# Optimization experiments

Hardware: AMD Instinct MI355X
Metric: run time of the kernel (lower is better)

Reference implementation:

```python
import jax, jax.numpy as jnp
import numpy as np

N = 8192          # num atoms
APM = 32          # atoms per molecule
M = N // APM      # 256 molecules
FEAT = 100        # hidden_channels == num_filters
NG = 25           # num gaussians
K = 28            # knn neighbors
L = 4             # num interaction blocks
CUTOFF = 6.0
LOG2 = float(np.log(2.0))


def ssp(x):
    # pyg ShiftedSoftplus: softplus(x) - log(2)
    return jax.nn.softplus(x) - LOG2


def setup_inputs() -> dict:
    key = jax.random.key(0)
    ks = jax.random.split(key, 16)
    z = jax.random.randint(ks[0], (N,), 1, 100)
    pos = jax.random.normal(ks[1], (N, 3), jnp.float32) * 2.0
    ptr = jnp.arange(0, N + APM, APM)  # [M+1] molecule boundaries

    def w(k, shape, fan):
        return (jax.random.normal(k, shape, jnp.float32) / np.sqrt(fan)).astype(jnp.float32)

    def b(k, shape):
        return jax.random.normal(k, shape, jnp.float32) * 0.01

    kb = jax.random.split(ks[15], 8)
    H = FEAT // 2
    return {
        "z": z,
        "pos": pos,
        "ptr": ptr,
        "emb": jax.random.normal(ks[2], (100, FEAT), jnp.float32),
        "mlp_w1": w(ks[3], (L, NG, FEAT), NG),
        "mlp_b1": b(kb[0], (L, FEAT)),
        "mlp_w2": w(ks[4], (L, FEAT, FEAT), FEAT),
        "mlp_b2": b(kb[1], (L, FEAT)),
        "lin1_w": w(ks[5], (L, FEAT, FEAT), FEAT),
        "lin2_w": w(ks[6], (L, FEAT, FEAT), FEAT),
        "lin2_b": b(kb[2], (L, FEAT)),
        "lin_w": w(ks[7], (L, FEAT, FEAT), FEAT),
        "lin_b": b(kb[3], (L, FEAT)),
        "out_w1": w(ks[8], (FEAT, H), FEAT),
        "out_b1": b(kb[4], (H,)),
        "out_w2": w(ks[9], (H, 1), H),
        "out_b2": b(kb[5], (1,)),
    }


def reference(z, pos, ptr, emb, mlp_w1, mlp_b1, mlp_w2, mlp_b2,
              lin1_w, lin2_w, lin2_b, lin_w, lin_b,
              out_w1, out_b1, out_w2, out_b2):
    n = z.shape[0]
    m = ptr.shape[0] - 1

    # ptr -> per-atom batch ids (index_fill + cumsum; OOB index N dropped)
    flag = jnp.zeros((n,), jnp.int32).at[ptr].set(1, mode="drop")
    flag = flag.at[0].set(0)
    batch = jnp.cumsum(flag)

    # ---- KNN interaction graph (full NxN pairwise distances + masking + topk)
    diff = pos[:, None, :] - pos[None, :, :]           # [N,N,3]
    d2 = jnp.sum(diff * diff, axis=-1)                  # [N,N]
    ar = jnp.arange(n)
    mask = (ar[:, None] == ar[None, :]) \
         | (batch[:, None] != batch[None, :]) \
         | (d2 > CUTOFF * CUTOFF)
    dist = jnp.where(mask, CUTOFF, jnp.sqrt(jnp.where(mask, 1.0, d2)))
    neg, idx = jax.lax.top_k(-dist, K)                  # k nearest per row
    ew = -neg.reshape(-1)                               # edge distances [N*K]
    src = idx.reshape(-1)                               # source atoms j; target of edge (i,m) is i

    # ---- Gaussian smearing
    offset = jnp.linspace(0.0, CUTOFF, NG)
    coeff = -0.5 / (offset[1] - offset[0]) ** 2
    ea = jnp.exp(coeff * (ew[:, None] - offset[None, :]) ** 2)  # [E,NG]

    # cosine cutoff (zero weight for padded edges at dist==cutoff)
    ccut = 0.5 * (jnp.cos(ew * jnp.pi / CUTOFF) + 1.0)          # [E]

    h = emb[z]                                                   # [N,F]
    f = h.shape[1]
    for l in range(L):
        # filter network on edge attributes
        Wf = ssp(ea @ mlp_w1[l] + mlp_b1[l]) @ mlp_w2[l] + mlp_b2[l]
        Wf = Wf * ccut[:, None]                                  # [E,F]
        # CFConv: lin1 -> gather*filter -> sum over k neighbors -> lin2
        x1 = h @ lin1_w[l]                                       # [N,F]
        msg = x1[src] * Wf                                       # [E,F]
        agg = msg.reshape(n, K, f).sum(axis=1)                   # each node i has exactly K incoming edges
        v = ssp(agg @ lin2_w[l] + lin2_b[l]) @ lin_w[l] + lin_b[l]
        h = h + v

    # readout head
    h = ssp(h @ out_w1 + out_b1)
    per_atom = (h @ out_w2 + out_b2).reshape(-1)                 # [N]
    return jax.ops.segment_sum(per_atom, batch, num_segments=m) # per-molecule energy [M]
```

## Files before the change

### kernel.cpp

```cpp
#include <hip/hip_runtime.h>
#include <math.h>

#define APM   32
#define NMOL  256
#define FEAT  100
#define NPAD  112
#define LAYERS 4
#define NTHREADS 1024
#define NWAVES   16
#define G_TBL 1024
#define TSTR  128
#define X1STR 132

typedef _Float16 f16x8 __attribute__((ext_vector_type(8)));
typedef float    f32x4 __attribute__((ext_vector_type(4)));

#define L1F_OFF 0
#define L2F_OFF 14336
#define LVF_OFF 28672
#define LWTOT   43008
#define WTOTAL  (4*LWTOT)

__device__ __forceinline__ float sspf(float x){
  return __logf(1.0f + __expf(x)) - 0.69314718056f;
}

__global__ __launch_bounds__(256) void prep_weights(
    const float* __restrict__ lin1_w, const float* __restrict__ lin2_w,
    const float* __restrict__ lin_w,  _Float16* __restrict__ out)
{
  int gid = blockIdx.x*256 + threadIdx.x;
  int l = gid / LWTOT;
  int r = gid - l*LWTOT;
  const float* W; int e;
  if (r < 14336)      { W = lin1_w + l*10000; e = r; }
  else if (r < 28672) { W = lin2_w + l*10000; e = r - 14336; }
  else                { W = lin_w  + l*10000; e = r - 28672; }
  int j = e & 7, L = (e >> 3) & 63, tile = e >> 9;
  int kc = tile / 7, nt = tile - kc*7;
  int k = kc*32 + ((L >> 4) << 3) + j;
  int f = nt*16 + (L & 15);
  float v = (k < 100 && f < FEAT) ? W[k*FEAT + f] : 0.0f;
  out[gid] = (_Float16)v;
}

__global__ __launch_bounds__(256) void build_table(
    const float* __restrict__ mlp_w1, const float* __restrict__ mlp_b1,
    const float* __restrict__ mlp_w2, const float* __restrict__ mlp_b2,
    float* __restrict__ tbl)
{
  __shared__ float sT[4][100];
  int wv = threadIdx.x >> 6, lane = threadIdx.x & 63;
  int l = blockIdx.x >> 8;
  int s = (blockIdx.x & 255)*4 + wv;
  float d = 6.0f * (float)s / (float)(G_TBL - 1);
  float ea[25];
  #pragma unroll
  for (int g = 0; g < 25; g++){
    float u = d - 0.25f*(float)g;
    ea[g] = __expf(-8.0f*u*u);
  }
  #pragma unroll
  for (int kk = 0; kk < 2; kk++){
    int k = lane + kk*64;
    if (k < 100){
      float acc = mlp_b1[l*100 + k];
      #pragma unroll
      for (int g = 0; g < 25; g++)
        acc += ea[g] * mlp_w1[(l*25 + g)*100 + k];
      sT[wv][k] = sspf(acc);
    }
  }
  float cc = 0.5f*(__cosf(d*0.52359877559f) + 1.0f);
  #pragma unroll
  for (int ff = 0; ff < 2; ff++){
    int f = lane + ff*64;
    float o = 0.0f;
    if (f < 100){
      o = mlp_b2[l*100 + f];
      for (int k = 0; k < 100; k++)
        o += sT[wv][k] * mlp_w2[(l*100 + k)*100 + f];
      o *= cc;
    }
    tbl[((size_t)l*G_TBL + s)*TSTR + f] = o;
  }
}

__device__ __forceinline__ void cpw(_Float16* dst, const _Float16* src, int n16){
  const uint4* s = (const uint4*)src;
  uint4* d = (uint4*)dst;
  for (int i = threadIdx.x; i < n16; i += NTHREADS) d[i] = s[i];
}

__global__ __launch_bounds__(1024)
__attribute__((amdgpu_waves_per_eu(4, 4)))
void schnet_mega(
    const int* __restrict__ z, const float* __restrict__ pos,
    const float* __restrict__ emb, const _Float16* __restrict__ wf,
    const float* __restrict__ tbl,
    const float* __restrict__ lin2_b, const float* __restrict__ lin_b,
    const float* __restrict__ out_w1, const float* __restrict__ out_b1,
    const float* __restrict__ out_w2, const float* __restrict__ out_b2,
    float* __restrict__ out)
{
  __shared__ __align__(16) _Float16 sWA[28672];
  __shared__ __align__(16) _Float16 sAf[APM*136];
  __shared__ __align__(16) _Float16 sBf[APM*136];
  __shared__ __align__(16) float    sX1[APM*X1STR];
  __shared__ __align__(16) float    sH [APM*NPAD];
  __shared__ float sD [APM*33];
  __shared__ float sM [APM*33];
  __shared__ float sB2l[NPAD], sBlv[NPAD];
  __shared__ float sPos[APM*3];
  __shared__ float sPart[NWAVES];

  int tid = threadIdx.x, lane = tid & 63, wv = tid >> 6;
  int q = lane >> 4, n = lane & 15;
  int mol = blockIdx.x, mb = mol*APM;

  if (tid < 96) sPos[tid] = pos[mb*3 + tid];
  if (tid < 512){
    int r0 = tid >> 4, c0 = 112 + (tid & 15);
    sBf[r0*136 + c0] = (_Float16)0.0f;
  }
  for (int i = tid; i < APM*NPAD; i += NTHREADS){
    int r = i/NPAD, c = i - r*NPAD;
    sH[i] = (c < FEAT) ? emb[z[mb+r]*FEAT + c] : 0.0f;
  }
  __syncthreads();
  for (int p = tid; p < APM*APM; p += NTHREADS){
    int i = p >> 5, j = p & 31;
    float dx = sPos[i*3+0]-sPos[j*3+0];
    float dy = sPos[i*3+1]-sPos[j*3+1];
    float dz = sPos[i*3+2]-sPos[j*3+2];
    float d2 = dx*dx + dy*dy + dz*dz;
    float d = (d2 > 36.0f) ? 6.0f : sqrtf(d2);
    sD[i*33+j] = d;
    sM[i*33+j] = 1.0f;
  }
  __syncthreads();
  if (tid < APM){
    float dd[32];
    #pragma unroll
    for (int j = 0; j < 32; j++) dd[j] = sD[tid*33+j];
    dd[tid] = 1e30f;
    unsigned dropped = 0u;
    for (int rr = 0; rr < 4; rr++){
      float mx = -1.0f; int mj = 0;
      #pragma unroll
      for (int j = 0; j < 32; j++){
        bool ok = !((dropped>>j)&1u) && (dd[j] > mx);
        mx = ok ? dd[j] : mx;  mj = ok ? j : mj;
      }
      dropped |= 1u << mj;
    }
    #pragma unroll
    for (int j = 0; j < 32; j++)
      if ((dropped>>j)&1u) sM[tid*33+j] = 0.0f;
  }
  __syncthreads();

  for (int l = 0; l < LAYERS; l++){
    const _Float16* wl = wf + l*LWTOT;
    const float* tb = tbl + (size_t)l*G_TBL*TSTR;
    cpw(sWA, wl + L1F_OFF, 14336/8);
    if (tid < 224){
      int w = tid/112, i = tid - w*112;
      float v = (i < FEAT) ? (w==0 ? lin2_b : lin_b)[l*FEAT + i] : 0.0f;
      (w==0 ? sB2l : sBlv)[i] = v;
    }
    for (int i = tid; i < APM*128; i += NTHREADS){
      int r = i >> 7, c = i & 127;
      sAf[r*136+c] = (c < NPAD) ? (_Float16)sH[r*NPAD+c] : (_Float16)0.0f;
    }
    __syncthreads();
    for (int tau = wv; tau < 14; tau += NWAVES){
      int mt = tau/7, nt = tau - mt*7;
      f32x4 acc = {0.0f,0.0f,0.0f,0.0f};
      #pragma unroll
      for (int kc = 0; kc < 4; kc++){
        f16x8 a = *(const f16x8*)&sAf[(mt*16+n)*136 + kc*32 + q*8];
        f16x8 b = *(const f16x8*)&sWA[((kc*7+nt)*64 + lane)*8];
        acc = __builtin_amdgcn_mfma_f32_16x16x32_f16(a, b, acc, 0, 0, 0);
      }
      #pragma unroll
      for (int r = 0; r < 4; r++)
        sX1[(mt*16+q*4+r)*X1STR + nt*16+n] = acc[r];
    }
    __syncthreads();
    cpw(sWA, wl + L2F_OFF, 28672/8);
    {
      #pragma unroll 1
      for (int t = 0; t < 2; t++){
        int a = wv*2 + t;
        int f0 = lane, f1 = lane + 64;
        float agg0 = 0.0f, agg1 = 0.0f;
        #pragma unroll 1
        for (int j0 = 0; j0 < 32; j0 += 4){
          float w00[4], w01[4], w10[4], w11[4], frv[4], mv[4];
          #pragma unroll
          for (int u = 0; u < 4; u++){
            int j = j0 + u;
            float d = sD[a*33+j];
            mv[u] = sM[a*33+j];
            float un = d * (float)((G_TBL-1)/6.0);
            int s = (int)un;
            s = (s > G_TBL-2) ? (G_TBL-2) : s;
            frv[u] = un - (float)s;
            const float* rp = tb + s*TSTR;
            w00[u] = rp[f0]; w01[u] = rp[TSTR+f0];
            w10[u] = rp[f1]; w11[u] = rp[TSTR+f1];
          }
          #pragma unroll
          for (int u = 0; u < 4; u++){
            int j = j0 + u;
            float wa = w00[u] + frv[u]*(w01[u]-w00[u]);
            float wb = w10[u] + frv[u]*(w11[u]-w10[u]);
            agg0 += (mv[u]*wa) * sX1[j*X1STR + f0];
            agg1 += (mv[u]*wb) * sX1[j*X1STR + f1];
          }
        }
        sAf[a*136 + f0] = (_Float16)agg0;
        sAf[a*136 + f1] = (_Float16)agg1;
      }
    }
    __syncthreads();
    for (int tau = wv; tau < 14; tau += NWAVES){
      int mt = tau/7, nt = tau - mt*7;
      f32x4 acc = {0.0f,0.0f,0.0f,0.0f};
      #pragma unroll
      for (int kc = 0; kc < 4; kc++){
        f16x8 a = *(const f16x8*)&sAf[(mt*16+n)*136 + kc*32 + q*8];
        f16x8 b = *(const f16x8*)&sWA[((kc*7+nt)*64 + lane)*8];
        acc = __builtin_amdgcn_mfma_f32_16x16x32_f16(a, b, acc, 0, 0, 0);
      }
      float bb = sB2l[nt*16+n];
      #pragma unroll
      for (int r = 0; r < 4; r++)
        sBf[(mt*16+q*4+r)*136 + nt*16+n] = (_Float16)sspf(acc[r] + bb);
    }
    __syncthreads();
    for (int tau = wv; tau < 14; tau += NWAVES){
      int mt = tau/7, nt = tau - mt*7;
      f32x4 acc = {0.0f,0.0f,0.0f,0.0f};
      #pragma unroll
      for (int kc = 0; kc < 4; kc++){
        f16x8 a = *(const f16x8*)&sBf[(mt*16+n)*136 + kc*32 + q*8];
        f16x8 b = *(const f16x8*)&sWA[14336 + ((kc*7+nt)*64 + lane)*8];
        acc = __builtin_amdgcn_mfma_f32_16x16x32_f16(a, b, acc, 0, 0, 0);
      }
      int f = nt*16 + n;
      if (f < FEAT){
        float bb = sBlv[f];
        #pragma unroll
        for (int r = 0; r < 4; r++)
          sH[(mt*16+q*4+r)*NPAD + f] += acc[r] + bb;
      }
    }
    __syncthreads();
  }

  float* rw = (float*)sWA;
  for (int i = tid; i < 5000; i += NTHREADS) rw[i] = out_w1[i];
  if (tid < 50){ sB2l[tid] = out_b1[tid]; sBlv[tid] = out_w2[tid]; }
  __syncthreads();
  float ob2 = out_b2[0];
  float partial = 0.0f;
  for (int t = 0; t < 2; t++){
    int a = wv*2 + t;
    float u = 0.0f;
    if (lane < 50){
      u = sB2l[lane];
      #pragma unroll 4
      for (int c = 0; c < FEAT; c++)
        u += sH[a*NPAD + c] * rw[c*50 + lane];
      u = sspf(u) * sBlv[lane];
    }
    #pragma unroll
    for (int s = 1; s < 64; s <<= 1) u += __shfl_xor(u, s);
    partial += u + ob2;
  }
  if (lane == 0) sPart[wv] = partial;
  __syncthreads();
  if (tid == 0){
    float s = 0.0f;
    #pragma unroll
    for (int i = 0; i < NWAVES; i++) s += sPart[i];
    out[mol] = s;
  }
}

extern "C" void kernel_launch(void* const* d_in, const int* in_sizes, int n_in,
                              void* d_out, int out_size, void* d_ws, size_t ws_size,
                              hipStream_t stream)
{
  const int*   z      = (const int*)  d_in[0];
  const float* pos    = (const float*)d_in[1];
  const float* emb    = (const float*)d_in[3];
  const float* mlp_w1 = (const float*)d_in[4];
  const float* mlp_b1 = (const float*)d_in[5];
  const float* mlp_w2 = (const float*)d_in[6];
  const float* mlp_b2 = (const float*)d_in[7];
  const float* lin1_w = (const float*)d_in[8];
  const float* lin2_w = (const float*)d_in[9];
  const float* lin2_b = (const float*)d_in[10];
  const float* lin_w  = (const float*)d_in[11];
  const float* lin_b  = (const float*)d_in[12];
  const float* out_w1 = (const float*)d_in[13];
  const float* out_b1 = (const float*)d_in[14];
  const float* out_w2 = (const float*)d_in[15];
  const float* out_b2 = (const float*)d_in[16];

  _Float16* wfrag = (_Float16*)d_ws;
  float*    tbl   = (float*)((char*)d_ws + WTOTAL*2);

  prep_weights<<<WTOTAL/256, 256, 0, stream>>>(lin1_w, lin2_w, lin_w, wfrag);
  build_table<<<4*(G_TBL/4), 256, 0, stream>>>(mlp_w1, mlp_b1, mlp_w2, mlp_b2,
                                               tbl);
  schnet_mega<<<NMOL, NTHREADS, 0, stream>>>(z, pos, emb, wfrag, tbl,
      lin2_b, lin_b, out_w1, out_b1, out_w2, out_b2, (float*)d_out);
}
```

Measured before the change: 166.1 us.

## Merge prep kernels, stage MLP weights in LDS, vectorize edge aggregation, drop mask array

The two setup kernels become one launch, and the filter-table builder loads mlp_w1/mlp_w2 into shared memory once per block, where before every thread read them from global memory. In the main kernel the neighbor mask is folded into the distance array by setting dropped edges to the cutoff distance, where the table value is zero. The aggregation loop processes two features per lane with float2 loads, and the fp16 copy of h is written in the layer epilogue instead of in a separate conversion pass. All three weight matrices share one enlarged LDS buffer, which raises shared-memory use per block.

```diff
diff --git a/kernel.cpp b/kernel.cpp
--- a/kernel.cpp
+++ b/kernel.cpp
@@ -13,7 +13,9 @@
 #define X1STR 132
 
 typedef _Float16 f16x8 __attribute__((ext_vector_type(8)));
+typedef _Float16 f16x2 __attribute__((ext_vector_type(2)));
 typedef float    f32x4 __attribute__((ext_vector_type(4)));
+typedef float    f32x2 __attribute__((ext_vector_type(2)));
 
 #define L1F_OFF 0
 #define L2F_OFF 14336
@@ -21,68 +23,83 @@
 #define LWTOT   43008
 #define WTOTAL  (4*LWTOT)
 
+#define PREP_BLOCKS 672
+#define TBL_BLOCKS  128
+
 __device__ __forceinline__ float sspf(float x){
   return __logf(1.0f + __expf(x)) - 0.69314718056f;
 }
 
-__global__ __launch_bounds__(256) void prep_weights(
+__global__ __launch_bounds__(256) void prep_all(
     const float* __restrict__ lin1_w, const float* __restrict__ lin2_w,
-    const float* __restrict__ lin_w,  _Float16* __restrict__ out)
-{
-  int gid = blockIdx.x*256 + threadIdx.x;
-  int l = gid / LWTOT;
-  int r = gid - l*LWTOT;
-  const float* W; int e;
-  if (r < 14336)      { W = lin1_w + l*10000; e = r; }
-  else if (r < 28672) { W = lin2_w + l*10000; e = r - 14336; }
-  else                { W = lin_w  + l*10000; e = r - 28672; }
-  int j = e & 7, L = (e >> 3) & 63, tile = e >> 9;
-  int kc = tile / 7, nt = tile - kc*7;
-  int k = kc*32 + ((L >> 4) << 3) + j;
-  int f = nt*16 + (L & 15);
-  float v = (k < 100 && f < FEAT) ? W[k*FEAT + f] : 0.0f;
-  out[gid] = (_Float16)v;
-}
-
-__global__ __launch_bounds__(256) void build_table(
+    const float* __restrict__ lin_w,
     const float* __restrict__ mlp_w1, const float* __restrict__ mlp_b1,
     const float* __restrict__ mlp_w2, const float* __restrict__ mlp_b2,
-    float* __restrict__ tbl)
+    _Float16* __restrict__ outw, float* __restrict__ tbl)
 {
+  if (blockIdx.x < PREP_BLOCKS){
+    int gid = blockIdx.x*256 + threadIdx.x;
+    int l = gid / LWTOT;
+    int r = gid - l*LWTOT;
+    const float* W; int e;
+    if (r < 14336)      { W = lin1_w + l*10000; e = r; }
+    else if (r < 28672) { W = lin2_w + l*10000; e = r - 14336; }
+    else                { W = lin_w  + l*10000; e = r - 28672; }
+    int j = e & 7, L = (e >> 3) & 63, tile = e >> 9;
+    int kc = tile / 7, nt = tile - kc*7;
+    int k = kc*32 + ((L >> 4) << 3) + j;
+    int f = nt*16 + (L & 15);
+    float v = (k < 100 && f < FEAT) ? W[k*FEAT + f] : 0.0f;
+    outw[gid] = (_Float16)v;
+    return;
+  }
+  __shared__ float sW2[10000];
+  __shared__ float sW1[2500];
+  __shared__ float sB1[100], sB2[100];
   __shared__ float sT[4][100];
-  int wv = threadIdx.x >> 6, lane = threadIdx.x & 63;
-  int l = blockIdx.x >> 8;
-  int s = (blockIdx.x & 255)*4 + wv;
-  float d = 6.0f * (float)s / (float)(G_TBL - 1);
-  float ea[25];
-  #pragma unroll
-  for (int g = 0; g < 25; g++){
-    float u = d - 0.25f*(float)g;
-    ea[g] = __expf(-8.0f*u*u);
-  }
-  #pragma unroll
-  for (int kk = 0; kk < 2; kk++){
-    int k = lane + kk*64;
-    if (k < 100){
-      float acc = mlp_b1[l*100 + k];
-      #pragma unroll
-      for (int g = 0; g < 25; g++)
-        acc += ea[g] * mlp_w1[(l*25 + g)*100 + k];
-      sT[wv][k] = sspf(acc);
-    }
-  }
-  float cc = 0.5f*(__cosf(d*0.52359877559f) + 1.0f);
-  #pragma unroll
-  for (int ff = 0; ff < 2; ff++){
-    int f = lane + ff*64;
-    float o = 0.0f;
-    if (f < 100){
-      o = mlp_b2[l*100 + f];
-      for (int k = 0; k < 100; k++)
-        o += sT[wv][k] * mlp_w2[(l*100 + k)*100 + f];
-      o *= cc;
-    }
-    tbl[((size_t)l*G_TBL + s)*TSTR + f] = o;
+  int bid = blockIdx.x - PREP_BLOCKS;
+  int l = bid >> 5;
+  int s0 = (bid & 31) * 32;
+  int tid = threadIdx.x, wv = tid >> 6, lane = tid & 63;
+  for (int i = tid; i < 10000; i += 256) sW2[i] = mlp_w2[l*10000 + i];
+  for (int i = tid; i < 2500;  i += 256) sW1[i] = mlp_w1[l*2500 + i];
+  if (tid < 100) sB1[tid] = mlp_b1[l*100 + tid];
+  if (tid >= 128 && tid < 228) sB2[tid-128] = mlp_b2[l*100 + tid-128];
+  __syncthreads();
+  #pragma unroll 1
+  for (int si = 0; si < 8; si++){
+    int s = s0 + wv*8 + si;
+    float d = 6.0f * (float)s / (float)(G_TBL - 1);
+    float ea[25];
+    #pragma unroll
+    for (int g = 0; g < 25; g++){
+      float u = d - 0.25f*(float)g;
+      ea[g] = __expf(-8.0f*u*u);
+    }
+    #pragma unroll
+    for (int kk = 0; kk < 2; kk++){
+      int k = lane + kk*64;
+      if (k < 100){
+        float acc = sB1[k];
+        #pragma unroll
+        for (int g = 0; g < 25; g++)
+          acc += ea[g] * sW1[g*100 + k];
+        sT[wv][k] = sspf(acc);
+      }
+    }
+    float cc = 0.5f*(__cosf(d*0.52359877559f) + 1.0f);
+    #pragma unroll
+    for (int ff = 0; ff < 2; ff++){
+      int f = lane + ff*64;
+      float o = 0.0f;
+      if (f < 100){
+        o = sB2[f];
+        for (int k = 0; k < 100; k++)
+          o += sT[wv][k] * sW2[k*100 + f];
+        o *= cc;
+      }
+      tbl[((size_t)l*G_TBL + s)*TSTR + f] = o;
+    }
   }
 }
 
@@ -103,13 +120,12 @@
     const float* __restrict__ out_w2, const float* __restrict__ out_b2,
     float* __restrict__ out)
 {
-  __shared__ __align__(16) _Float16 sWA[28672];
+  __shared__ __align__(16) _Float16 sWA[43008];
   __shared__ __align__(16) _Float16 sAf[APM*136];
   __shared__ __align__(16) _Float16 sBf[APM*136];
   __shared__ __align__(16) float    sX1[APM*X1STR];
   __shared__ __align__(16) float    sH [APM*NPAD];
   __shared__ float sD [APM*33];
-  __shared__ float sM [APM*33];
   __shared__ float sB2l[NPAD], sBlv[NPAD];
   __shared__ float sPos[APM*3];
   __shared__ float sPart[NWAVES];
@@ -123,9 +139,16 @@
     int r0 = tid >> 4, c0 = 112 + (tid & 15);
     sBf[r0*136 + c0] = (_Float16)0.0f;
   }
-  for (int i = tid; i < APM*NPAD; i += NTHREADS){
-    int r = i/NPAD, c = i - r*NPAD;
-    sH[i] = (c < FEAT) ? emb[z[mb+r]*FEAT + c] : 0.0f;
+  if (tid >= 512 && tid < 512 + APM*20){
+    int i = tid - 512;
+    int r = i/20, c = 112 + (i - r*20);
+    sX1[r*X1STR + c] = 0.0f;
+  }
+  for (int i = tid; i < APM*136; i += NTHREADS){
+    int r = i/136, c = i - r*136;
+    float v = (c < FEAT) ? emb[z[mb+r]*FEAT + c] : 0.0f;
+    sAf[i] = (_Float16)v;
+    if (c < NPAD) sH[r*NPAD + c] = v;
   }
   __syncthreads();
   for (int p = tid; p < APM*APM; p += NTHREADS){
@@ -134,9 +157,7 @@
     float dy = sPos[i*3+1]-sPos[j*3+1];
     float dz = sPos[i*3+2]-sPos[j*3+2];
     float d2 = dx*dx + dy*dy + dz*dz;
-    float d = (d2 > 36.0f) ? 6.0f : sqrtf(d2);
-    sD[i*33+j] = d;
-    sM[i*33+j] = 1.0f;
+    sD[i*33+j] = (d2 > 36.0f) ? 6.0f : sqrtf(d2);
   }
   __syncthreads();
   if (tid < APM){
@@ -156,7 +177,7 @@
     }
     #pragma unroll
     for (int j = 0; j < 32; j++)
-      if ((dropped>>j)&1u) sM[tid*33+j] = 0.0f;
+      if ((dropped>>j)&1u) sD[tid*33+j] = 6.0f;
   }
   __syncthreads();
 
@@ -169,10 +190,6 @@
       float v = (i < FEAT) ? (w==0 ? lin2_b : lin_b)[l*FEAT + i] : 0.0f;
       (w==0 ? sB2l : sBlv)[i] = v;
     }
-    for (int i = tid; i < APM*128; i += NTHREADS){
-      int r = i >> 7, c = i & 127;
-      sAf[r*136+c] = (c < NPAD) ? (_Float16)sH[r*NPAD+c] : (_Float16)0.0f;
-    }
     __syncthreads();
     for (int tau = wv; tau < 14; tau += NWAVES){
       int mt = tau/7, nt = tau - mt*7;
@@ -188,40 +205,41 @@
         sX1[(mt*16+q*4+r)*X1STR + nt*16+n] = acc[r];
     }
     __syncthreads();
-    cpw(sWA, wl + L2F_OFF, 28672/8);
+    cpw(sWA + 14336, wl + L2F_OFF, 28672/8);
     {
+      int fb = 2*lane;
+      const float* rpb = tb + fb;
       #pragma unroll 1
       for (int t = 0; t < 2; t++){
         int a = wv*2 + t;
-        int f0 = lane, f1 = lane + 64;
-        float agg0 = 0.0f, agg1 = 0.0f;
-        #pragma unroll 1
-        for (int j0 = 0; j0 < 32; j0 += 4){
-          float w00[4], w01[4], w10[4], w11[4], frv[4], mv[4];
-          #pragma unroll
-          for (int u = 0; u < 4; u++){
-            int j = j0 + u;
-            float d = sD[a*33+j];
-            mv[u] = sM[a*33+j];
-            float un = d * (float)((G_TBL-1)/6.0);
-            int s = (int)un;
-            s = (s > G_TBL-2) ? (G_TBL-2) : s;
-            frv[u] = un - (float)s;
-            const float* rp = tb + s*TSTR;
-            w00[u] = rp[f0]; w01[u] = rp[TSTR+f0];
-            w10[u] = rp[f1]; w11[u] = rp[TSTR+f1];
+        if (lane < 56){
+          f32x2 agg = {0.0f, 0.0f};
+          #pragma unroll 1
+          for (int j0 = 0; j0 < 32; j0 += 4){
+            float frv[4]; f32x2 w0[4], w1[4];
+            #pragma unroll
+            for (int u = 0; u < 4; u++){
+              float d = sD[a*33 + j0 + u];
+              float un = d * (float)((G_TBL-1)/6.0);
+              int s = (int)un;
+              s = (s > G_TBL-2) ? (G_TBL-2) : s;
+              frv[u] = un - (float)s;
+              const float* rp = rpb + s*TSTR;
+              w0[u] = *(const f32x2*)rp;
+              w1[u] = *(const f32x2*)(rp + TSTR);
+            }
+            #pragma unroll
+            for (int u = 0; u < 4; u++){
+              f32x2 w = w0[u] + frv[u]*(w1[u] - w0[u]);
+              f32x2 x = *(const f32x2*)&sX1[(j0+u)*X1STR + fb];
+              agg += w * x;
+            }
           }
-          #pragma unroll
-          for (int u = 0; u < 4; u++){
-            int j = j0 + u;
-            float wa = w00[u] + frv[u]*(w01[u]-w00[u]);
-            float wb = w10[u] + frv[u]*(w11[u]-w10[u]);
-            agg0 += (mv[u]*wa) * sX1[j*X1STR + f0];
-            agg1 += (mv[u]*wb) * sX1[j*X1STR + f1];
-          }
+          *(f16x2*)&sAf[a*136 + fb] =
+              (f16x2){(_Float16)agg.x, (_Float16)agg.y};
+        } else {
+          *(f16x2*)&sAf[a*136 + fb] = (f16x2){(_Float16)0.0f, (_Float16)0.0f};
         }
-        sAf[a*136 + f0] = (_Float16)agg0;
-        sAf[a*136 + f1] = (_Float16)agg1;
       }
     }
     __syncthreads();
@@ -231,7 +249,7 @@
       #pragma unroll
       for (int kc = 0; kc < 4; kc++){
         f16x8 a = *(const f16x8*)&sAf[(mt*16+n)*136 + kc*32 + q*8];
-        f16x8 b = *(const f16x8*)&sWA[((kc*7+nt)*64 + lane)*8];
+        f16x8 b = *(const f16x8*)&sWA[14336 + ((kc*7+nt)*64 + lane)*8];
         acc = __builtin_amdgcn_mfma_f32_16x16x32_f16(a, b, acc, 0, 0, 0);
       }
       float bb = sB2l[nt*16+n];
@@ -246,15 +264,19 @@
       #pragma unroll
       for (int kc = 0; kc < 4; kc++){
         f16x8 a = *(const f16x8*)&sBf[(mt*16+n)*136 + kc*32 + q*8];
-        f16x8 b = *(const f16x8*)&sWA[14336 + ((kc*7+nt)*64 + lane)*8];
+        f16x8 b = *(const f16x8*)&sWA[28672 + ((kc*7+nt)*64 + lane)*8];
         acc = __builtin_amdgcn_mfma_f32_16x16x32_f16(a, b, acc, 0, 0, 0);
       }
       int f = nt*16 + n;
       if (f < FEAT){
         float bb = sBlv[f];
         #pragma unroll
-        for (int r = 0; r < 4; r++)
-          sH[(mt*16+q*4+r)*NPAD + f] += acc[r] + bb;
+        for (int r = 0; r < 4; r++){
+          int row = mt*16 + q*4 + r;
+          float hn = sH[row*NPAD + f] + acc[r] + bb;
+          sH[row*NPAD + f] = hn;
+          sAf[row*136 + f] = (_Float16)hn;
+        }
       }
     }
     __syncthreads();
@@ -314,9 +336,8 @@
   _Float16* wfrag = (_Float16*)d_ws;
   float*    tbl   = (float*)((char*)d_ws + WTOTAL*2);
 
-  prep_weights<<<WTOTAL/256, 256, 0, stream>>>(lin1_w, lin2_w, lin_w, wfrag);
-  build_table<<<4*(G_TBL/4), 256, 0, stream>>>(mlp_w1, mlp_b1, mlp_w2, mlp_b2,
-                                               tbl);
+  prep_all<<<PREP_BLOCKS + TBL_BLOCKS, 256, 0, stream>>>(
+      lin1_w, lin2_w, lin_w, mlp_w1, mlp_b1, mlp_w2, mlp_b2, wfrag, tbl);
   schnet_mega<<<NMOL, NTHREADS, 0, stream>>>(z, pos, emb, wfrag, tbl,
       lin2_b, lin_b, out_w1, out_b1, out_w2, out_b2, (float*)d_out);
 }
```

After: 201.4 us. 21.3% more time.
